# Kernel tuning notes

Hardware: AMD Instinct MI355X
Metric: run time of the kernel (lower is better)

The kernel has to match this reference:

```python
import jax, jax.numpy as jnp
from jax import lax
import numpy as np

SEQ_LEN, BATCH, INPUT_SIZE, HIDDEN_SIZE = 1024, 64, 512, 512


def setup_inputs() -> dict:
    key = jax.random.key(0)
    k1, k2, k3 = jax.random.split(key, 3)
    inputs = jax.random.normal(k1, (SEQ_LEN, BATCH, INPUT_SIZE), dtype=jnp.float32)
    # nn.Linear(input_size + hidden_size, hidden_size): W [H, I+H], b [H]
    fan_in = INPUT_SIZE + HIDDEN_SIZE
    bound = 1.0 / np.sqrt(fan_in)
    W = jax.random.uniform(k2, (HIDDEN_SIZE, fan_in), minval=-bound, maxval=bound, dtype=jnp.float32)
    b = jax.random.uniform(k3, (HIDDEN_SIZE,), minval=-bound, maxval=bound, dtype=jnp.float32)
    return {"inputs": inputs, "W": W, "b": b}


def reference(inputs, W, b):
    # inputs: [T, B, I]; hidden starts at zeros [B, H]
    hidden_size = W.shape[0]
    # Split W into hidden part and input part to avoid per-step concat:
    # layer_input = cat(h, x) -> y = h @ Wh^T + x @ Wx^T + b
    Wh = W[:, :hidden_size]          # [H, H]
    Wx = W[:, hidden_size:]          # [H, I]
    h0 = jnp.zeros((inputs.shape[1], hidden_size), dtype=inputs.dtype)

    def step(h, x):
        h_new = jnp.tanh(h @ Wh.T + x @ Wx.T + b)
        return h_new, None

    h_final, _ = lax.scan(step, h0, inputs)
    return h_final
```

## Files before the change

kernel.cpp:

```cpp
#include <hip/hip_runtime.h>


#define SEQ 1024
#define NB  64
#define HID 512

typedef _Float16 half2v __attribute__((ext_vector_type(2)));
typedef _Float16 f16x8  __attribute__((ext_vector_type(8)));
typedef float    f32x4  __attribute__((ext_vector_type(4)));

#if __has_builtin(__builtin_amdgcn_fdot2)
#define DOT2(a, b, c) __builtin_amdgcn_fdot2((a), (b), (c), false)
#else
static __device__ __forceinline__ float DOT2(half2v a, half2v b, float c) {
  return c + (float)a.x * (float)b.x + (float)a.y * (float)b.y;
}
#endif

static __device__ __forceinline__ float fast_tanh(float x) {
  float e = __expf(2.0f * x);
  return (e - 1.0f) / (e + 1.0f);
}

__global__ __launch_bounds__(256, 2)
void rnn_prepass(const float* __restrict__ X, const float* __restrict__ W,
                 const float* __restrict__ bias, _Float16* __restrict__ U) {
  __shared__ __align__(16) _Float16 As[128][40];
  __shared__ __align__(16) _Float16 Bs[128][40];
  const int tid = threadIdx.x;
  const int m0 = blockIdx.x * 128;
  const int n0 = blockIdx.y * 128;
  const int wave = tid >> 6, lane = tid & 63;
  const int wm = (wave >> 1) * 64, wn = (wave & 1) * 64;
  const int l15 = lane & 15, q = lane >> 4;

  f32x4 acc[4][4];
#pragma unroll
  for (int i = 0; i < 4; ++i)
#pragma unroll
    for (int j = 0; j < 4; ++j) acc[i][j] = (f32x4){0.f, 0.f, 0.f, 0.f};

  const int srow = tid >> 1;
  const int shalf = (tid & 1) * 16;

  for (int k0 = 0; k0 < 512; k0 += 32) {
    const float* asrc = X + (size_t)(m0 + srow) * 512 + k0 + shalf;
    const float* bsrc = W + (size_t)(n0 + srow) * 1024 + 512 + k0 + shalf;
    float4 a0 = *(const float4*)(asrc);
    float4 a1 = *(const float4*)(asrc + 4);
    float4 a2 = *(const float4*)(asrc + 8);
    float4 a3 = *(const float4*)(asrc + 12);
    float4 b0 = *(const float4*)(bsrc);
    float4 b1 = *(const float4*)(bsrc + 4);
    float4 b2 = *(const float4*)(bsrc + 8);
    float4 b3 = *(const float4*)(bsrc + 12);
    __syncthreads();
    f16x8 pa0 = {(_Float16)a0.x, (_Float16)a0.y, (_Float16)a0.z, (_Float16)a0.w,
                 (_Float16)a1.x, (_Float16)a1.y, (_Float16)a1.z, (_Float16)a1.w};
    f16x8 pa1 = {(_Float16)a2.x, (_Float16)a2.y, (_Float16)a2.z, (_Float16)a2.w,
                 (_Float16)a3.x, (_Float16)a3.y, (_Float16)a3.z, (_Float16)a3.w};
    f16x8 pb0 = {(_Float16)b0.x, (_Float16)b0.y, (_Float16)b0.z, (_Float16)b0.w,
                 (_Float16)b1.x, (_Float16)b1.y, (_Float16)b1.z, (_Float16)b1.w};
    f16x8 pb1 = {(_Float16)b2.x, (_Float16)b2.y, (_Float16)b2.z, (_Float16)b2.w,
                 (_Float16)b3.x, (_Float16)b3.y, (_Float16)b3.z, (_Float16)b3.w};
    *(f16x8*)&As[srow][shalf] = pa0;
    *(f16x8*)&As[srow][shalf + 8] = pa1;
    *(f16x8*)&Bs[srow][shalf] = pb0;
    *(f16x8*)&Bs[srow][shalf + 8] = pb1;
    __syncthreads();
    f16x8 av[4], bv[4];
#pragma unroll
    for (int i = 0; i < 4; ++i)
      av[i] = *(const f16x8*)&As[wm + i * 16 + l15][q * 8];
#pragma unroll
    for (int j = 0; j < 4; ++j)
      bv[j] = *(const f16x8*)&Bs[wn + j * 16 + l15][q * 8];
#pragma unroll
    for (int i = 0; i < 4; ++i)
#pragma unroll
      for (int j = 0; j < 4; ++j)
        acc[i][j] = __builtin_amdgcn_mfma_f32_16x16x32_f16(av[i], bv[j], acc[i][j], 0, 0, 0);
  }
  float bj[4];
#pragma unroll
  for (int j = 0; j < 4; ++j) bj[j] = bias[n0 + wn + j * 16 + l15];
#pragma unroll
  for (int i = 0; i < 4; ++i)
#pragma unroll
    for (int j = 0; j < 4; ++j)
#pragma unroll
      for (int r = 0; r < 4; ++r) {
        int m = m0 + wm + i * 16 + q * 4 + r;
        int n = n0 + wn + j * 16 + l15;
        U[(size_t)m * 512 + n] = (_Float16)(acc[i][j][r] + bj[j]);
      }
}

__global__ __launch_bounds__(256, 1)
void rnn_recur(const float* __restrict__ W, const _Float16* __restrict__ U,
               unsigned long long* hbuf, float* __restrict__ out) {
  const int blk = blockIdx.x;
  const int batch = blk & 63;
  const int g = blk >> 6;
  const int tid = threadIdx.x;
  const int wvi = tid >> 6;
  const int l   = tid & 63;
  const int jj  = l >> 3;
  const int c   = l & 7;
  const int rg  = wvi * 8 + jj;

  __shared__ __align__(16) unsigned char hmem[8 * 144];

  f16x8 wreg[32];
#pragma unroll
  for (int i = 0; i < 4; ++i) {
    const float* wrow = W + (size_t)(128 * g + 4 * rg + i) * 1024 + 64 * c;
#pragma unroll
    for (int q = 0; q < 8; ++q) {
      float4 wa = *(const float4*)(wrow + 8 * q);
      float4 wb = *(const float4*)(wrow + 8 * q + 4);
      f16x8 p = {(_Float16)wa.x, (_Float16)wa.y, (_Float16)wa.z, (_Float16)wa.w,
                 (_Float16)wb.x, (_Float16)wb.y, (_Float16)wb.z, (_Float16)wb.w};
      wreg[i * 8 + q] = p;
    }
  }

  const unsigned int* ubase = (const unsigned int*)U;
  unsigned long long* hb = hbuf + (size_t)batch * 256;

  const bool puber = (c < 2);
  const int wpub = 2 * rg + c;
  const int wid  = g * 64 + wpub;

  float h0f = 0.f, h1f = 0.f;
  for (int t = 0; t < SEQ; ++t) {
    unsigned int ubits = 0;
    if (puber)
      ubits = ubase[((size_t)t * NB + batch) * 256 + wid];

    {
      const unsigned long long* src = hb + (size_t)(t & 1) * (NB * 256) + tid;
      unsigned long long e;
      do {
        e = __hip_atomic_load(src, __ATOMIC_RELAXED, __HIP_MEMORY_SCOPE_AGENT);
      } while ((unsigned int)(e >> 32) != (unsigned int)t);
      *(unsigned int*)(hmem + (tid >> 5) * 144 + (tid & 31) * 4) = (unsigned int)e;
    }
    __syncthreads();

    float a[4] = {0.f, 0.f, 0.f, 0.f};
    const unsigned char* hc = hmem + c * 144;
#pragma unroll
    for (int q = 0; q < 8; ++q) {
      f16x8 hv = *(const f16x8*)(hc + 16 * q);
      half2v h0 = {hv[0], hv[1]}, h1 = {hv[2], hv[3]},
             h2 = {hv[4], hv[5]}, h3 = {hv[6], hv[7]};
#pragma unroll
      for (int i = 0; i < 4; ++i) {
        f16x8 wv = wreg[i * 8 + q];
        half2v w0 = {wv[0], wv[1]}, w1 = {wv[2], wv[3]},
               w2 = {wv[4], wv[5]}, w3 = {wv[6], wv[7]};
        a[i] = DOT2(w0, h0, a[i]);
        a[i] = DOT2(w1, h1, a[i]);
        a[i] = DOT2(w2, h2, a[i]);
        a[i] = DOT2(w3, h3, a[i]);
      }
    }
#pragma unroll
    for (int m = 1; m <= 4; m <<= 1) {
#pragma unroll
      for (int i = 0; i < 4; ++i) a[i] += __shfl_xor(a[i], m, 64);
    }

    if (puber) {
      half2v uh = __builtin_bit_cast(half2v, ubits);
      float s0 = (c == 0) ? a[0] : a[2];
      float s1 = (c == 0) ? a[1] : a[3];
      h0f = fast_tanh(s0 + (float)uh.x);
      h1f = fast_tanh(s1 + (float)uh.y);
      half2v hh;
      hh.x = (_Float16)h0f;
      hh.y = (_Float16)h1f;
      unsigned long long word =
          ((unsigned long long)(unsigned int)(t + 1) << 32) |
          (unsigned long long)__builtin_bit_cast(unsigned int, hh);
      __hip_atomic_store(hb + (size_t)((t + 1) & 1) * (NB * 256) + wid, word,
                         __ATOMIC_RELAXED, __HIP_MEMORY_SCOPE_AGENT);
    }
    __syncthreads();
  }
  if (puber) {
    out[(size_t)batch * HID + 128 * g + 2 * wpub]     = h0f;
    out[(size_t)batch * HID + 128 * g + 2 * wpub + 1] = h1f;
  }
}

extern "C" void kernel_launch(void* const* d_in, const int* in_sizes, int n_in,
                              void* d_out, int out_size, void* d_ws, size_t ws_size,
                              hipStream_t stream) {
  const float* X    = (const float*)d_in[0];
  const float* W    = (const float*)d_in[1];
  const float* bias = (const float*)d_in[2];
  float* out = (float*)d_out;

  char* ws = (char*)d_ws;
  _Float16* U = (_Float16*)ws;
  unsigned long long* hbuf =
      (unsigned long long*)(ws + (size_t)SEQ * NB * HID * 2);

  hipMemsetAsync(hbuf, 0, (size_t)NB * 256 * 8, stream);

  rnn_prepass<<<dim3(512, 4), dim3(256), 0, stream>>>(X, W, bias, U);

  const float* Wp = W;
  const _Float16* Up = U;
  unsigned long long* hb = hbuf;
  float* op = out;
  void* args[] = {(void*)&Wp, (void*)&Up, (void*)&hb, (void*)&op};
  hipError_t e = hipLaunchCooperativeKernel(
      reinterpret_cast<void*>(rnn_recur), dim3(256), dim3(256), args, 0, stream);
  if (e != hipSuccess) {
    rnn_recur<<<dim3(256), dim3(256), 0, stream>>>(Wp, Up, hb, op);
  }
}
```

Baseline: 1.526 ms.

## Double-buffer hidden LDS, pipeline spin-polls, use DPP reductions in recurrence

```diff
diff --git a/kernel.cpp b/kernel.cpp
--- a/kernel.cpp
+++ b/kernel.cpp
@@ -21,6 +21,16 @@
   float e = __expf(2.0f * x);
   return (e - 1.0f) / (e + 1.0f);
 }
+
+template <int CTRL>
+static __device__ __forceinline__ float dpp_add(float v) {
+  int s = __builtin_bit_cast(int, v);
+  int p = __builtin_amdgcn_update_dpp(0, s, CTRL, 0xF, 0xF, true);
+  return v + __builtin_bit_cast(float, p);
+}
+#define DPP_QUAD_XOR1 0xB1
+#define DPP_QUAD_XOR2 0x4E
+#define DPP_HALF_MIRR 0x141
 
 __global__ __launch_bounds__(256, 2)
 void rnn_prepass(const float* __restrict__ X, const float* __restrict__ W,
@@ -28,8 +38,8 @@
   __shared__ __align__(16) _Float16 As[128][40];
   __shared__ __align__(16) _Float16 Bs[128][40];
   const int tid = threadIdx.x;
-  const int m0 = blockIdx.x * 128;
-  const int n0 = blockIdx.y * 128;
+  const int m0 = blockIdx.y * 128;
+  const int n0 = blockIdx.x * 128;
   const int wave = tid >> 6, lane = tid & 63;
   const int wm = (wave >> 1) * 64, wn = (wave & 1) * 64;
   const int l15 = lane & 15, q = lane >> 4;
@@ -109,7 +119,7 @@
   const int c   = l & 7;
   const int rg  = wvi * 8 + jj;
 
-  __shared__ __align__(16) unsigned char hmem[8 * 144];
+  __shared__ __align__(16) unsigned char hmem[2][8 * 144];
 
   f16x8 wreg[32];
 #pragma unroll
@@ -140,16 +150,29 @@
 
     {
       const unsigned long long* src = hb + (size_t)(t & 1) * (NB * 256) + tid;
+      const unsigned int want = (unsigned int)t;
+      unsigned long long e0 = __hip_atomic_load(src, __ATOMIC_RELAXED, __HIP_MEMORY_SCOPE_AGENT);
+      unsigned long long e1 = __hip_atomic_load(src, __ATOMIC_RELAXED, __HIP_MEMORY_SCOPE_AGENT);
+      unsigned long long e2 = __hip_atomic_load(src, __ATOMIC_RELAXED, __HIP_MEMORY_SCOPE_AGENT);
+      unsigned long long e3 = __hip_atomic_load(src, __ATOMIC_RELAXED, __HIP_MEMORY_SCOPE_AGENT);
       unsigned long long e;
-      do {
-        e = __hip_atomic_load(src, __ATOMIC_RELAXED, __HIP_MEMORY_SCOPE_AGENT);
-      } while ((unsigned int)(e >> 32) != (unsigned int)t);
-      *(unsigned int*)(hmem + (tid >> 5) * 144 + (tid & 31) * 4) = (unsigned int)e;
+      for (;;) {
+        if ((unsigned int)(e0 >> 32) == want) { e = e0; break; }
+        e0 = __hip_atomic_load(src, __ATOMIC_RELAXED, __HIP_MEMORY_SCOPE_AGENT);
+        if ((unsigned int)(e1 >> 32) == want) { e = e1; break; }
+        e1 = __hip_atomic_load(src, __ATOMIC_RELAXED, __HIP_MEMORY_SCOPE_AGENT);
+        if ((unsigned int)(e2 >> 32) == want) { e = e2; break; }
+        e2 = __hip_atomic_load(src, __ATOMIC_RELAXED, __HIP_MEMORY_SCOPE_AGENT);
+        if ((unsigned int)(e3 >> 32) == want) { e = e3; break; }
+        e3 = __hip_atomic_load(src, __ATOMIC_RELAXED, __HIP_MEMORY_SCOPE_AGENT);
+      }
+      *(unsigned int*)(hmem[t & 1] + (tid >> 5) * 144 + (tid & 31) * 4) =
+          (unsigned int)e;
     }
     __syncthreads();
 
     float a[4] = {0.f, 0.f, 0.f, 0.f};
-    const unsigned char* hc = hmem + c * 144;
+    const unsigned char* hc = hmem[t & 1] + c * 144;
 #pragma unroll
     for (int q = 0; q < 8; ++q) {
       f16x8 hv = *(const f16x8*)(hc + 16 * q);
@@ -167,10 +190,11 @@
       }
     }
 #pragma unroll
-    for (int m = 1; m <= 4; m <<= 1) {
-#pragma unroll
-      for (int i = 0; i < 4; ++i) a[i] += __shfl_xor(a[i], m, 64);
-    }
+    for (int i = 0; i < 4; ++i) a[i] = dpp_add<DPP_QUAD_XOR1>(a[i]);
+#pragma unroll
+    for (int i = 0; i < 4; ++i) a[i] = dpp_add<DPP_QUAD_XOR2>(a[i]);
+#pragma unroll
+    for (int i = 0; i < 4; ++i) a[i] = dpp_add<DPP_HALF_MIRR>(a[i]);
 
     if (puber) {
       half2v uh = __builtin_bit_cast(half2v, ubits);
@@ -187,7 +211,6 @@
       __hip_atomic_store(hb + (size_t)((t + 1) & 1) * (NB * 256) + wid, word,
                          __ATOMIC_RELAXED, __HIP_MEMORY_SCOPE_AGENT);
     }
-    __syncthreads();
   }
   if (puber) {
     out[(size_t)batch * HID + 128 * g + 2 * wpub]     = h0f;
@@ -208,9 +231,9 @@
   unsigned long long* hbuf =
       (unsigned long long*)(ws + (size_t)SEQ * NB * HID * 2);
 
-  hipMemsetAsync(hbuf, 0, (size_t)NB * 256 * 8, stream);
-
-  rnn_prepass<<<dim3(512, 4), dim3(256), 0, stream>>>(X, W, bias, U);
+  (void)hipMemsetAsync(hbuf, 0, (size_t)NB * 256 * 8, stream);
+
+  rnn_prepass<<<dim3(4, 512), dim3(256), 0, stream>>>(X, W, bias, U);
 
   const float* Wp = W;
   const _Float16* Up = U;
```

After: 1.771 ms. 1.16x slower.
